# Optimization experiments

Measured on AMD Instinct MI355X. Metric: run time of the kernel, lower is better.

The kernel has to match this reference:

```python
import jax, jax.numpy as jnp
import numpy as np

EPS = 1e-5

def layernorm(x, g, b):
    mu = jnp.mean(x, axis=-1, keepdims=True)
    var = jnp.mean(jnp.square(x - mu), axis=-1, keepdims=True)
    return (x - mu) * jax.lax.rsqrt(var + EPS) * g + b

def rope(x):
    # x: [B, H, S, hd]; faithful to source: theta = 10000**(-2*pos/hd), pos in {0,2,4,...}
    S, hd = x.shape[-2], x.shape[-1]
    pos2 = jnp.arange(0, hd, 2, dtype=jnp.float32)
    theta = jnp.power(10000.0, -2.0 * pos2 / hd)          # [hd/2]
    ang = jnp.arange(S, dtype=jnp.float32)[:, None] * theta  # [S, hd/2]
    cos, sin = jnp.cos(ang), jnp.sin(ang)                  # broadcast over B,H
    xr = x.reshape(*x.shape[:-1], hd // 2, 2)
    x0, x1 = xr[..., 0], xr[..., 1]
    out = jnp.stack([x0 * cos - x1 * sin, x1 * cos + x0 * sin], axis=-1)
    return out.reshape(x.shape)

def setup_inputs() -> dict:
    key = jax.random.key(0)
    ks = jax.random.split(key, 8)
    B, S, D, H = 2, 2048, 1024, 16
    hd = D // H
    s_in = 1.0 / np.sqrt(D)
    s_h = 1.0 / np.sqrt(2 * D)
    return {
        "x": jax.random.normal(ks[0], (B, S, D), jnp.float32),
        "ln1_g": jnp.ones((D,), jnp.float32),
        "ln1_b": jnp.zeros((D,), jnp.float32),
        "Wq": jax.random.normal(ks[1], (H, D, hd), jnp.float32) * s_in,
        "Wk": jax.random.normal(ks[2], (H, D, hd), jnp.float32) * s_in,
        "Wv": jax.random.normal(ks[3], (H, D, hd), jnp.float32) * s_in,
        "Wo": jax.random.normal(ks[4], (D, D), jnp.float32) * s_in,
        "ln2_g": jnp.ones((D,), jnp.float32),
        "ln2_b": jnp.zeros((D,), jnp.float32),
        "W1": jax.random.normal(ks[5], (D, 2 * D), jnp.float32) * s_in,
        "W2": jax.random.normal(ks[6], (D, 2 * D), jnp.float32) * s_in,
        "W3": jax.random.normal(ks[7], (2 * D, D), jnp.float32) * s_h,
    }

def reference(x, ln1_g, ln1_b, Wq, Wk, Wv, Wo, ln2_g, ln2_b, W1, W2, W3):
    B, S, D = x.shape
    # --- attention sublayer ---
    h = layernorm(x, ln1_g, ln1_b)
    q = jnp.einsum("bsd,hdk->bhsk", h, Wq)
    k = jnp.einsum("bsd,hdk->bhsk", h, Wk)
    v = jnp.einsum("bsd,hdk->bhsk", h, Wv)
    q, k = rope(q), rope(k)
    hd = q.shape[-1]
    scores = jnp.einsum("bhqk,bhsk->bhqs", q, k) * (hd ** -0.5)  # [B,H,S,S]
    causal = jnp.tril(jnp.ones((S, S), bool))
    scores = jnp.where(causal, scores, jnp.float32(-jnp.inf))
    attn = jax.nn.softmax(scores, axis=-1)
    o = jnp.einsum("bhqs,bhsk->bhqk", attn, v)                   # [B,H,S,hd]
    o = o.transpose(0, 2, 1, 3).reshape(B, S, D)                 # concat heads
    x = x + o @ Wo
    # --- SwiGLU FFN sublayer ---
    h2 = layernorm(x, ln2_g, ln2_b)
    u = h2 @ W1
    ffn = (u * jax.nn.sigmoid(u)) * (h2 @ W2)
    return x + ffn @ W3
```

## Files before the change

### kernel.cpp

```cpp
#include <hip/hip_runtime.h>
#include <hip/hip_bf16.h>

using bf16 = __hip_bfloat16;
typedef __attribute__((ext_vector_type(8))) short bf16x8;
typedef __attribute__((ext_vector_type(4))) float f32x4;


__device__ inline float toF(float x) { return x; }
__device__ inline float toF(bf16 x) { return __bfloat162float(x); }
__device__ inline void  stV(float* p, float v) { *p = v; }
__device__ inline void  stV(bf16* p, float v) { *p = __float2bfloat16(v); }

__device__ __forceinline__ void unpack8(uint4 u, float* f) {
    f[0] = __uint_as_float(u.x << 16); f[1] = __uint_as_float(u.x & 0xffff0000u);
    f[2] = __uint_as_float(u.y << 16); f[3] = __uint_as_float(u.y & 0xffff0000u);
    f[4] = __uint_as_float(u.z << 16); f[5] = __uint_as_float(u.z & 0xffff0000u);
    f[6] = __uint_as_float(u.w << 16); f[7] = __uint_as_float(u.w & 0xffff0000u);
}

__device__ __forceinline__ uint4 packbf8(const float* f) {
    union { unsigned short u[8]; uint4 v; } r;
#pragma unroll
    for (int i = 0; i < 8; i++) {
        bf16 b = __float2bfloat16(f[i]);
        r.u[i] = *(unsigned short*)&b;
    }
    return r.v;
}

__device__ __forceinline__ unsigned pack2(float lo, float hi) {
    bf16 a = __float2bfloat16(lo), b = __float2bfloat16(hi);
    return ((unsigned)*(unsigned short*)&b << 16) | (unsigned)*(unsigned short*)&a;
}

__device__ __forceinline__ void gl_lds16(const void* g, void* l) {
    __builtin_amdgcn_global_load_lds(
        (__attribute__((address_space(1))) void*)g,
        (__attribute__((address_space(3))) void*)l, 16, 0, 0);
}

template <typename Tx, typename To>
__global__ __launch_bounds__(256) void ln_kernel(
    const Tx* __restrict__ x, const float* __restrict__ g,
    const float* __restrict__ b, To* __restrict__ out)
{
    const int D = 1024;
    int row = blockIdx.x;
    int tid = threadIdx.x;
    const Tx* xr = x + (size_t)row * D;

    float vals[4];
    float sum = 0.f, sumsq = 0.f;
#pragma unroll
    for (int i = 0; i < 4; i++) {
        float v = toF(xr[tid + i * 256]);
        vals[i] = v; sum += v; sumsq += v * v;
    }
#pragma unroll
    for (int off = 32; off > 0; off >>= 1) {
        sum += __shfl_xor(sum, off);
        sumsq += __shfl_xor(sumsq, off);
    }
    __shared__ float s1[4], s2[4];
    int wave = tid >> 6, lane = tid & 63;
    if (lane == 0) { s1[wave] = sum; s2[wave] = sumsq; }
    __syncthreads();
    sum = s1[0] + s1[1] + s1[2] + s1[3];
    sumsq = s2[0] + s2[1] + s2[2] + s2[3];

    float mu = sum * (1.f / D);
    float var = sumsq * (1.f / D) - mu * mu;
    float rstd = rsqrtf(var + 1e-5f);

    To* orow = out + (size_t)row * D;
#pragma unroll
    for (int i = 0; i < 4; i++) {
        int c = tid + i * 256;
        stV(&orow[c], (vals[i] - mu) * rstd * g[c] + b[c]);
    }
}

__global__ __launch_bounds__(256) void tconv_kernel(
    const float* __restrict__ in, bf16* __restrict__ out, int R, int C)
{
    __shared__ float t[32][33];
    int hh = blockIdx.z;
    const float* ip = in + (size_t)hh * R * C;
    bf16* op = out + (size_t)hh * R * C;
    int c0 = blockIdx.x * 32, r0 = blockIdx.y * 32;
    int tx = threadIdx.x & 31, ty = threadIdx.x >> 5;
#pragma unroll
    for (int i = 0; i < 4; i++)
        t[ty + 8 * i][tx] = ip[(size_t)(r0 + ty + 8 * i) * C + c0 + tx];
    __syncthreads();
#pragma unroll
    for (int i = 0; i < 4; i++)
        op[(size_t)(c0 + ty + 8 * i) * R + r0 + tx] = __float2bfloat16(t[tx][ty + 8 * i]);
}

__global__ __launch_bounds__(256) void tconv_w_kernel(
    const float* __restrict__ Aq, const float* __restrict__ Ak,
    const float* __restrict__ Av, const float* __restrict__ Ao,
    bf16* __restrict__ out)
{
    __shared__ float t[32][33];
    int z = blockIdx.z;
    const float* ip; int ldi;
    if (z < 48) {
        const float* s = (z < 16) ? Aq : (z < 32) ? Ak : Av;
        ip = s + (size_t)(z & 15) * 65536; ldi = 64;
    } else {
        ip = Ao + (size_t)(z - 48) * 64; ldi = 1024;
    }
    bf16* op = out + ((size_t)z << 16);
    int c0 = blockIdx.x * 32, r0 = blockIdx.y * 32;
    int tx = threadIdx.x & 31, ty = threadIdx.x >> 5;
#pragma unroll
    for (int i = 0; i < 4; i++)
        t[ty + 8 * i][tx] = ip[(size_t)(r0 + ty + 8 * i) * ldi + c0 + tx];
    __syncthreads();
#pragma unroll
    for (int i = 0; i < 4; i++)
        op[(size_t)(c0 + ty + 8 * i) * 1024 + r0 + tx] = __float2bfloat16(t[tx][ty + 8 * i]);
}

__global__ __launch_bounds__(256) void tconv12_kernel(
    const float* __restrict__ W1, const float* __restrict__ W2,
    bf16* __restrict__ out)
{
    __shared__ float t[32][33];
    int z = blockIdx.z;
    const float* ip = z ? W2 : W1;
    bf16* op = out + ((size_t)z << 21);
    int c0 = blockIdx.x * 32, r0 = blockIdx.y * 32;
    int tx = threadIdx.x & 31, ty = threadIdx.x >> 5;
#pragma unroll
    for (int i = 0; i < 4; i++)
        t[ty + 8 * i][tx] = ip[(size_t)(r0 + ty + 8 * i) * 2048 + c0 + tx];
    __syncthreads();
#pragma unroll
    for (int i = 0; i < 4; i++)
        op[(size_t)(c0 + ty + 8 * i) * 1024 + r0 + tx] = __float2bfloat16(t[tx][ty + 8 * i]);
}

template <int MODE>
__global__ __launch_bounds__(256) void mfma_gemm(
    const bf16* __restrict__ A, const bf16* __restrict__ BT0,
    void* __restrict__ Cv, const void* __restrict__ resv,
    int M, int N, int K)
{
    constexpr int NB = (MODE == 5) ? 3 : 2;
    __shared__ bf16 smem[2][NB][64 * 64];
    int tid = threadIdx.x, lane = tid & 63, w = tid >> 6;
    int wm = w >> 1, wn = w & 1;
    int m0 = blockIdx.y * 64, n0 = blockIdx.x * 64;

    const bf16* BT = BT0;
    bf16* Cq = nullptr; int rope = 0;
    if (MODE == 1) {
        int z = blockIdx.z;
        BT = BT0 + ((size_t)z << 20);
        Cq = (bf16*)Cv + ((size_t)z << 21);
        rope = (z < 2);
    }

    int lrow = lane >> 3;
    int lcb  = (lane & 7) ^ lrow;
    const bf16* Ag  = A  + (size_t)(m0 + w * 8 + lrow) * K + lcb * 8;
    const bf16* Bg0 = BT + (size_t)(n0 + w * 8 + lrow) * K + lcb * 8;
    const bf16* B2g = (MODE == 5)
        ? (const bf16*)resv + (size_t)(n0 + w * 8 + lrow) * K + lcb * 8
        : nullptr;
    unsigned sbase = (unsigned)__builtin_amdgcn_readfirstlane(w * 8 * 128);
    char* smc = (char*)smem;

    f32x4 acc[2][2], acc2[2][2];
#pragma unroll
    for (int i = 0; i < 2; i++)
#pragma unroll
        for (int j = 0; j < 2; j++) {
            acc[i][j] = (f32x4){0.f, 0.f, 0.f, 0.f};
            if (MODE == 5) acc2[i][j] = (f32x4){0.f, 0.f, 0.f, 0.f};
        }

    int cidx = lane & 15, quad = lane >> 4;

    auto STAGE = [&](int buf, int k0) {
        char* p = smc + (size_t)buf * (NB * 8192) + sbase;
        gl_lds16(Ag + k0,                   p);
        gl_lds16(Ag + (size_t)32 * K + k0,  p + 4096);
        gl_lds16(Bg0 + k0,                  p + 8192);
        gl_lds16(Bg0 + (size_t)32 * K + k0, p + 12288);
        if (MODE == 5) {
            gl_lds16(B2g + k0,                  p + 16384);
            gl_lds16(B2g + (size_t)32 * K + k0, p + 20480);
        }
    };

    STAGE(0, 0);
    __syncthreads();
    int cur = 0;
    for (int k0 = 0; k0 < K; k0 += 64) {
        if (k0 + 64 < K) STAGE(cur ^ 1, k0 + 64);
        const bf16* Ab = (const bf16*)(smc + (size_t)cur * (NB * 8192));
        const bf16* Bb = Ab + 4096;
        const bf16* B2b = Ab + 8192;
#pragma unroll
        for (int kk = 0; kk < 2; kk++) {
            int pb = (kk * 4 + quad) ^ (cidx & 7);
            bf16x8 af[2], bfr[2], b2f[2];
#pragma unroll
            for (int i = 0; i < 2; i++)
                af[i] = *(const bf16x8*)&Ab[(wm * 32 + i * 16 + cidx) * 64 + pb * 8];
#pragma unroll
            for (int j = 0; j < 2; j++)
                bfr[j] = *(const bf16x8*)&Bb[(wn * 32 + j * 16 + cidx) * 64 + pb * 8];
            if (MODE == 5) {
#pragma unroll
                for (int j = 0; j < 2; j++)
                    b2f[j] = *(const bf16x8*)&B2b[(wn * 32 + j * 16 + cidx) * 64 + pb * 8];
            }
            __builtin_amdgcn_s_setprio(1);
#pragma unroll
            for (int i = 0; i < 2; i++)
#pragma unroll
                for (int j = 0; j < 2; j++) {
                    acc[i][j] = __builtin_amdgcn_mfma_f32_16x16x32_bf16(af[i], bfr[j], acc[i][j], 0, 0, 0);
                    if (MODE == 5)
                        acc2[i][j] = __builtin_amdgcn_mfma_f32_16x16x32_bf16(af[i], b2f[j], acc2[i][j], 0, 0, 0);
                }
            __builtin_amdgcn_s_setprio(0);
        }
        __syncthreads();
        cur ^= 1;
    }

    int rbase = quad * 4;
#pragma unroll
    for (int i = 0; i < 2; i++) {
#pragma unroll
        for (int j = 0; j < 2; j++) {
            int row0 = m0 + wm * 32 + i * 16 + rbase;
            int col = n0 + wn * 32 + j * 16 + cidx;
            if (MODE == 1 && !rope) {
                int h_ = col >> 6, d = col & 63;
                uint2 t;
                t.x = pack2(acc[i][j][0], acc[i][j][1]);
                t.y = pack2(acc[i][j][2], acc[i][j][3]);
                *(uint2*)&Cq[(size_t)h_ * 131072 + (size_t)d * 2048 + row0] = t;
                continue;
            }
#pragma unroll
            for (int r = 0; r < 4; r++) {
                int row = row0 + r;
                float v = acc[i][j][r];
                size_t idx = (size_t)row * N + col;
                if (MODE == 1) {
                    int h_ = col >> 6, kk = col & 63;
                    float other = __shfl_xor(v, 1);
                    float p = (float)(kk >> 1);
                    float theta = __expf(p * -0.5756462732485114f);
                    float ang = (float)row * theta;
                    float c, sn; __sincosf(ang, &sn, &c);
                    float outv = (kk & 1) ? (v * c + other * sn) : (v * c - other * sn);
                    Cq[((size_t)h_ * 2048 + row) * 64 + kk] = __float2bfloat16(outv);
                } else if (MODE == 2) {
                    v += ((const float*)resv)[idx];
                    ((bf16*)Cv)[idx] = __float2bfloat16(v);
                } else if (MODE == 5) {
                    float g2 = acc2[i][j][r];
                    float sg = 1.f / (1.f + __expf(-v));
                    ((bf16*)Cv)[idx] = __float2bfloat16(v * sg * g2);
                } else {
                    v += __bfloat162float(((const bf16*)resv)[idx]);
                    ((float*)Cv)[idx] = v;
                }
            }
        }
    }
}

__global__ __launch_bounds__(256) void attn_kernel(
    const bf16* __restrict__ q, const bf16* __restrict__ k,
    const bf16* __restrict__ vt, bf16* __restrict__ o)
{
    const int S = 2048;
    __shared__ bf16 Ks[64][72];
    __shared__ bf16 Vs[64][72];
    __shared__ __align__(16) char QPbuf[64 * 72 * 2];

    int h = blockIdx.y;
    int qt = (h & 8) ? (int)blockIdx.x : 31 - (int)blockIdx.x;
    int tid = threadIdx.x, lane = tid & 63, w = tid >> 6;
    int quad = lane >> 4, cidx = lane & 15;
    int m0 = qt * 64;

    const bf16* qb = q + ((size_t)h * S + m0) * 64;
    const bf16* kb = k + (size_t)h * S * 64;
    const bf16* vtb = vt + (size_t)h * 64 * S;

    int srow = tid >> 2;
    int sg = (tid & 3) * 16;

    bf16 (*Qs)[72] = (bf16 (*)[72])QPbuf;
    {
        const uint4* src = (const uint4*)(qb + (size_t)srow * 64 + sg);
        uint4 u0 = src[0], u1 = src[1];
        float f[16]; unpack8(u0, f); unpack8(u1, f + 8);
#pragma unroll
        for (int i = 0; i < 16; i++) f[i] *= 0.125f * 1.44269504f;
        *(uint4*)&Qs[srow][sg] = packbf8(f);
        *(uint4*)&Qs[srow][sg + 8] = packbf8(f + 8);
    }
    bf16x8 bQ0 = *(const bf16x8*)&Qs[w * 16 + cidx][quad * 8];
    bf16x8 bQ1 = *(const bf16x8*)&Qs[w * 16 + cidx][32 + quad * 8];

    unsigned* Pst = (unsigned*)QPbuf + w * 576;

    float m_i = -INFINITY, l_i = 0.f;
    f32x4 Oc[4];
#pragma unroll
    for (int i = 0; i < 4; i++) Oc[i] = (f32x4){0.f, 0.f, 0.f, 0.f};

    uint4 ka0, ka1, va0, va1;
    {
        const uint4* ksrc = (const uint4*)(kb + (size_t)srow * 64 + sg);
        ka0 = ksrc[0]; ka1 = ksrc[1];
        const uint4* vsrc = (const uint4*)(vtb + (size_t)srow * S + sg);
        va0 = vsrc[0]; va1 = vsrc[1];
    }

    for (int kt = 0; kt <= qt; kt++) {
        __syncthreads();
        *(uint4*)&Ks[srow][sg] = ka0; *(uint4*)&Ks[srow][sg + 8] = ka1;
        *(uint4*)&Vs[srow][sg] = va0; *(uint4*)&Vs[srow][sg + 8] = va1;
        __syncthreads();
        if (kt < qt) {
            const uint4* kn = (const uint4*)(kb + (size_t)((kt + 1) * 64 + srow) * 64 + sg);
            ka0 = kn[0]; ka1 = kn[1];
            const uint4* vn = (const uint4*)(vtb + (size_t)srow * S + (kt + 1) * 64 + sg);
            va0 = vn[0]; va1 = vn[1];
        }

        f32x4 sc[4];
#pragma unroll
        for (int i = 0; i < 4; i++) {
            bf16x8 aK0 = *(const bf16x8*)&Ks[i * 16 + cidx][quad * 8];
            bf16x8 aK1 = *(const bf16x8*)&Ks[i * 16 + cidx][32 + quad * 8];
            f32x4 z = (f32x4){0.f, 0.f, 0.f, 0.f};
            z = __builtin_amdgcn_mfma_f32_16x16x32_bf16(aK0, bQ0, z, 0, 0, 0);
            z = __builtin_amdgcn_mfma_f32_16x16x32_bf16(aK1, bQ1, z, 0, 0, 0);
            sc[i] = z;
        }

        if (kt == qt) {
#pragma unroll
            for (int i = 0; i < 4; i++)
#pragma unroll
                for (int r = 0; r < 4; r++)
                    if (i * 16 + quad * 4 + r > w * 16 + cidx) sc[i][r] = -INFINITY;
        }

        float pmax = sc[0][0];
#pragma unroll
        for (int i = 0; i < 4; i++)
#pragma unroll
            for (int r = 0; r < 4; r++) pmax = fmaxf(pmax, sc[i][r]);
        pmax = fmaxf(pmax, __shfl_xor(pmax, 16));
        pmax = fmaxf(pmax, __shfl_xor(pmax, 32));
        float mnew = fmaxf(m_i, pmax);
        float alpha = __builtin_amdgcn_exp2f(m_i - mnew);
        float rs = 0.f;
#pragma unroll
        for (int i = 0; i < 4; i++)
#pragma unroll
            for (int r = 0; r < 4; r++) {
                sc[i][r] = __builtin_amdgcn_exp2f(sc[i][r] - mnew);
                rs += sc[i][r];
            }
        rs += __shfl_xor(rs, 16);
        rs += __shfl_xor(rs, 32);
        l_i = l_i * alpha + rs;
        m_i = mnew;
#pragma unroll
        for (int i = 0; i < 4; i++) {
            Oc[i][0] *= alpha; Oc[i][1] *= alpha;
            Oc[i][2] *= alpha; Oc[i][3] *= alpha;
        }

#pragma unroll
        for (int i = 0; i < 4; i++) {
            uint2 t;
            t.x = pack2(sc[i][0], sc[i][1]);
            t.y = pack2(sc[i][2], sc[i][3]);
            *(uint2*)&Pst[cidx * 36 + 8 * i + 2 * quad] = t;
        }
        bf16x8 bP0 = *(const bf16x8*)&Pst[cidx * 36 + 4 * quad];
        bf16x8 bP1 = *(const bf16x8*)&Pst[cidx * 36 + 16 + 4 * quad];

#pragma unroll
        for (int i = 0; i < 4; i++) {
            bf16x8 aV0 = *(const bf16x8*)&Vs[i * 16 + cidx][quad * 8];
            bf16x8 aV1 = *(const bf16x8*)&Vs[i * 16 + cidx][32 + quad * 8];
            Oc[i] = __builtin_amdgcn_mfma_f32_16x16x32_bf16(aV0, bP0, Oc[i], 0, 0, 0);
            Oc[i] = __builtin_amdgcn_mfma_f32_16x16x32_bf16(aV1, bP1, Oc[i], 0, 0, 0);
        }
    }

    float inv = 1.f / l_i;
#pragma unroll
    for (int i = 0; i < 4; i++) {
        uint2 t;
        t.x = pack2(Oc[i][0] * inv, Oc[i][1] * inv);
        t.y = pack2(Oc[i][2] * inv, Oc[i][3] * inv);
        *(uint2*)&Pst[cidx * 36 + 8 * i + 2 * quad] = t;
    }
    int r2 = lane >> 2, g2 = (lane & 3) * 8;
    uint4 o0 = *(const uint4*)&Pst[r2 * 36 + g2];
    uint4 o1 = *(const uint4*)&Pst[r2 * 36 + g2 + 4];
    bf16* orow = o + (size_t)(m0 + w * 16 + r2) * 1024 + h * 64;
    *(uint4*)(orow + g2 * 2) = o0;
    *(uint4*)(orow + g2 * 2 + 8) = o1;
}

extern "C" void kernel_launch(void* const* d_in, const int* in_sizes, int n_in,
                              void* d_out, int out_size, void* d_ws, size_t ws_size,
                              hipStream_t stream)
{
    const int S = 2048, D = 1024;

    const float* x    = (const float*)d_in[0];
    const float* ln1g = (const float*)d_in[1];
    const float* ln1b = (const float*)d_in[2];
    const float* Wq   = (const float*)d_in[3];
    const float* Wk   = (const float*)d_in[4];
    const float* Wv   = (const float*)d_in[5];
    const float* Wo   = (const float*)d_in[6];
    const float* ln2g = (const float*)d_in[7];
    const float* ln2b = (const float*)d_in[8];
    const float* W1   = (const float*)d_in[9];
    const float* W2   = (const float*)d_in[10];
    const float* W3   = (const float*)d_in[11];
    float* out = (float*)d_out;

    const size_t NR = (size_t)S * D;
    bf16* r0 = (bf16*)d_ws;
    bf16* r1 = r0 + NR;
    bf16* r2 = r1 + NR;
    bf16* r3 = r2 + NR;
    const size_t M1 = 1u << 20;

    for (int b = 0; b < 2; b++) {
        const float* xb = x + (size_t)b * S * D;
        float* ob = out + (size_t)b * S * D;
        bf16* pb = (bf16*)ob;

        ln_kernel<float, bf16><<<S, 256, 0, stream>>>(xb, ln1g, ln1b, r3);

        tconv_w_kernel<<<dim3(2, 32, 64), 256, 0, stream>>>(Wq, Wk, Wv, Wo, pb);

        mfma_gemm<1><<<dim3(16, 32, 3), 256, 0, stream>>>(r3, pb, r0, nullptr, S, 1024, 1024);

        attn_kernel<<<dim3(32, 16), 256, 0, stream>>>(r0, r1, r2, pb);

        mfma_gemm<2><<<dim3(16, 32, 1), 256, 0, stream>>>(pb, pb + 3 * M1, r3, xb, S, 1024, 1024);

        ln_kernel<bf16, bf16><<<S, 256, 0, stream>>>(r3, ln2g, ln2b, r0);

        tconv12_kernel<<<dim3(64, 32, 2), 256, 0, stream>>>(W1, W2, pb);

        mfma_gemm<5><<<dim3(32, 32, 1), 256, 0, stream>>>(r0, pb, r1, pb + 2 * M1, S, 2048, 1024);

        tconv_kernel<<<dim3(32, 64, 1), 256, 0, stream>>>(W3, r0, 2048, 1024);

        mfma_gemm<4><<<dim3(16, 32, 1), 256, 0, stream>>>(r1, r0, ob, r3, S, 1024, 2048);
    }
}
```

Before: 368.9 us.

## Widen attention key tile to 128 and fuse layernorm with weight conversion

The attention kernel now handles 128 keys per iteration instead of 64. This doubles the K/V shared-memory tiles and the P staging buffer, roughly halves the loop trip count and the barriers per query tile, and still applies the causal mask on the last tile. Separately, each layernorm launch is merged with its weight transpose/convert launch into one kernel that picks its role by block index, cutting the launch count. The costs are more shared memory per attention block, which may lower occupancy, and some masked waste on the final 128-wide tile for query tiles with even index.

```diff
diff --git a/kernel.cpp b/kernel.cpp
--- a/kernel.cpp
+++ b/kernel.cpp
@@ -8,8 +8,6 @@
 
 __device__ inline float toF(float x) { return x; }
 __device__ inline float toF(bf16 x) { return __bfloat162float(x); }
-__device__ inline void  stV(float* p, float v) { *p = v; }
-__device__ inline void  stV(bf16* p, float v) { *p = __float2bfloat16(v); }
 
 __device__ __forceinline__ void unpack8(uint4 u, float* f) {
     f[0] = __uint_as_float(u.x << 16); f[1] = __uint_as_float(u.x & 0xffff0000u);
@@ -39,13 +37,13 @@
         (__attribute__((address_space(3))) void*)l, 16, 0, 0);
 }
 
-template <typename Tx, typename To>
-__global__ __launch_bounds__(256) void ln_kernel(
+template <typename Tx>
+__device__ __forceinline__ void ln_body(
     const Tx* __restrict__ x, const float* __restrict__ g,
-    const float* __restrict__ b, To* __restrict__ out)
+    const float* __restrict__ b, bf16* __restrict__ out, int row,
+    float* s1, float* s2)
 {
     const int D = 1024;
-    int row = blockIdx.x;
     int tid = threadIdx.x;
     const Tx* xr = x + (size_t)row * D;
 
@@ -61,7 +59,6 @@
         sum += __shfl_xor(sum, off);
         sumsq += __shfl_xor(sumsq, off);
     }
-    __shared__ float s1[4], s2[4];
     int wave = tid >> 6, lane = tid & 63;
     if (lane == 0) { s1[wave] = sum; s2[wave] = sumsq; }
     __syncthreads();
@@ -72,21 +69,84 @@
     float var = sumsq * (1.f / D) - mu * mu;
     float rstd = rsqrtf(var + 1e-5f);
 
-    To* orow = out + (size_t)row * D;
+    bf16* orow = out + (size_t)row * D;
 #pragma unroll
     for (int i = 0; i < 4; i++) {
         int c = tid + i * 256;
-        stV(&orow[c], (vals[i] - mu) * rstd * g[c] + b[c]);
-    }
+        orow[c] = __float2bfloat16((vals[i] - mu) * rstd * g[c] + b[c]);
+    }
+}
+
+__global__ __launch_bounds__(256) void prep1_kernel(
+    const float* __restrict__ x, const float* __restrict__ g,
+    const float* __restrict__ b, bf16* __restrict__ h,
+    const float* __restrict__ Wq, const float* __restrict__ Wk,
+    const float* __restrict__ Wv, const float* __restrict__ Wo,
+    bf16* __restrict__ wt)
+{
+    __shared__ float t[32][33];
+    __shared__ float s1[4], s2[4];
+    int bx = blockIdx.x;
+    if (bx < 2048) {
+        ln_body<float>(x, g, b, h, bx, s1, s2);
+        return;
+    }
+    int zz = bx - 2048;
+    int z = zz >> 6, rem = zz & 63;
+    int yy = rem >> 1, xx = rem & 1;
+    const float* ip; int ldi;
+    if (z < 48) {
+        const float* s = (z < 16) ? Wq : (z < 32) ? Wk : Wv;
+        ip = s + (size_t)(z & 15) * 65536; ldi = 64;
+    } else {
+        ip = Wo + (size_t)(z - 48) * 64; ldi = 1024;
+    }
+    bf16* op = wt + ((size_t)z << 16);
+    int c0 = xx * 32, r0 = yy * 32;
+    int tx = threadIdx.x & 31, ty = threadIdx.x >> 5;
+#pragma unroll
+    for (int i = 0; i < 4; i++)
+        t[ty + 8 * i][tx] = ip[(size_t)(r0 + ty + 8 * i) * ldi + c0 + tx];
+    __syncthreads();
+#pragma unroll
+    for (int i = 0; i < 4; i++)
+        op[(size_t)(c0 + ty + 8 * i) * 1024 + r0 + tx] = __float2bfloat16(t[tx][ty + 8 * i]);
+}
+
+__global__ __launch_bounds__(256) void prep2_kernel(
+    const bf16* __restrict__ x2, const float* __restrict__ g,
+    const float* __restrict__ b, bf16* __restrict__ h2,
+    const float* __restrict__ W1, const float* __restrict__ W2,
+    bf16* __restrict__ wt)
+{
+    __shared__ float t[32][33];
+    __shared__ float s1[4], s2[4];
+    int bx = blockIdx.x;
+    if (bx < 2048) {
+        ln_body<bf16>(x2, g, b, h2, bx, s1, s2);
+        return;
+    }
+    int zz = bx - 2048;
+    int xx = zz & 63, yy = (zz >> 6) & 31, z = zz >> 11;
+    const float* ip = z ? W2 : W1;
+    bf16* op = wt + ((size_t)z << 21);
+    int c0 = xx * 32, r0 = yy * 32;
+    int tx = threadIdx.x & 31, ty = threadIdx.x >> 5;
+#pragma unroll
+    for (int i = 0; i < 4; i++)
+        t[ty + 8 * i][tx] = ip[(size_t)(r0 + ty + 8 * i) * 2048 + c0 + tx];
+    __syncthreads();
+#pragma unroll
+    for (int i = 0; i < 4; i++)
+        op[(size_t)(c0 + ty + 8 * i) * 1024 + r0 + tx] = __float2bfloat16(t[tx][ty + 8 * i]);
 }
 
 __global__ __launch_bounds__(256) void tconv_kernel(
     const float* __restrict__ in, bf16* __restrict__ out, int R, int C)
 {
     __shared__ float t[32][33];
-    int hh = blockIdx.z;
-    const float* ip = in + (size_t)hh * R * C;
-    bf16* op = out + (size_t)hh * R * C;
+    const float* ip = in;
+    bf16* op = out;
     int c0 = blockIdx.x * 32, r0 = blockIdx.y * 32;
     int tx = threadIdx.x & 31, ty = threadIdx.x >> 5;
 #pragma unroll
@@ -96,51 +156,6 @@
 #pragma unroll
     for (int i = 0; i < 4; i++)
         op[(size_t)(c0 + ty + 8 * i) * R + r0 + tx] = __float2bfloat16(t[tx][ty + 8 * i]);
-}
-
-__global__ __launch_bounds__(256) void tconv_w_kernel(
-    const float* __restrict__ Aq, const float* __restrict__ Ak,
-    const float* __restrict__ Av, const float* __restrict__ Ao,
-    bf16* __restrict__ out)
-{
-    __shared__ float t[32][33];
-    int z = blockIdx.z;
-    const float* ip; int ldi;
-    if (z < 48) {
-        const float* s = (z < 16) ? Aq : (z < 32) ? Ak : Av;
-        ip = s + (size_t)(z & 15) * 65536; ldi = 64;
-    } else {
-        ip = Ao + (size_t)(z - 48) * 64; ldi = 1024;
-    }
-    bf16* op = out + ((size_t)z << 16);
-    int c0 = blockIdx.x * 32, r0 = blockIdx.y * 32;
-    int tx = threadIdx.x & 31, ty = threadIdx.x >> 5;
-#pragma unroll
-    for (int i = 0; i < 4; i++)
-        t[ty + 8 * i][tx] = ip[(size_t)(r0 + ty + 8 * i) * ldi + c0 + tx];
-    __syncthreads();
-#pragma unroll
-    for (int i = 0; i < 4; i++)
-        op[(size_t)(c0 + ty + 8 * i) * 1024 + r0 + tx] = __float2bfloat16(t[tx][ty + 8 * i]);
-}
-
-__global__ __launch_bounds__(256) void tconv12_kernel(
-    const float* __restrict__ W1, const float* __restrict__ W2,
-    bf16* __restrict__ out)
-{
-    __shared__ float t[32][33];
-    int z = blockIdx.z;
-    const float* ip = z ? W2 : W1;
-    bf16* op = out + ((size_t)z << 21);
-    int c0 = blockIdx.x * 32, r0 = blockIdx.y * 32;
-    int tx = threadIdx.x & 31, ty = threadIdx.x >> 5;
-#pragma unroll
-    for (int i = 0; i < 4; i++)
-        t[ty + 8 * i][tx] = ip[(size_t)(r0 + ty + 8 * i) * 2048 + c0 + tx];
-    __syncthreads();
-#pragma unroll
-    for (int i = 0; i < 4; i++)
-        op[(size_t)(c0 + ty + 8 * i) * 1024 + r0 + tx] = __float2bfloat16(t[tx][ty + 8 * i]);
 }
 
 template <int MODE>
@@ -285,9 +300,9 @@
     const bf16* __restrict__ vt, bf16* __restrict__ o)
 {
     const int S = 2048;
-    __shared__ bf16 Ks[64][72];
-    __shared__ bf16 Vs[64][72];
-    __shared__ __align__(16) char QPbuf[64 * 72 * 2];
+    __shared__ bf16 Ks[128][72];
+    __shared__ bf16 Vs[64][136];
+    __shared__ __align__(16) char QPbuf[4 * 16 * 272];
 
     int h = blockIdx.y;
     int qt = (h & 8) ? (int)blockIdx.x : 31 - (int)blockIdx.x;
@@ -300,7 +315,8 @@
     const bf16* vtb = vt + (size_t)h * 64 * S;
 
     int srow = tid >> 2;
-    int sg = (tid & 3) * 16;
+    int sg  = (tid & 3) * 16;
+    int sg2 = (tid & 3) * 32;
 
     bf16 (*Qs)[72] = (bf16 (*)[72])QPbuf;
     {
@@ -315,36 +331,42 @@
     bf16x8 bQ0 = *(const bf16x8*)&Qs[w * 16 + cidx][quad * 8];
     bf16x8 bQ1 = *(const bf16x8*)&Qs[w * 16 + cidx][32 + quad * 8];
 
-    unsigned* Pst = (unsigned*)QPbuf + w * 576;
+    unsigned* Pst = (unsigned*)QPbuf + w * (16 * 68);
 
     float m_i = -INFINITY, l_i = 0.f;
     f32x4 Oc[4];
 #pragma unroll
     for (int i = 0; i < 4; i++) Oc[i] = (f32x4){0.f, 0.f, 0.f, 0.f};
 
-    uint4 ka0, ka1, va0, va1;
+    int nt = qt / 2 + 1;
+
+    uint4 ka[4], va[4];
     {
-        const uint4* ksrc = (const uint4*)(kb + (size_t)srow * 64 + sg);
-        ka0 = ksrc[0]; ka1 = ksrc[1];
-        const uint4* vsrc = (const uint4*)(vtb + (size_t)srow * S + sg);
-        va0 = vsrc[0]; va1 = vsrc[1];
-    }
-
-    for (int kt = 0; kt <= qt; kt++) {
+        const uint4* k0 = (const uint4*)(kb + (size_t)srow * 64 + sg);
+        const uint4* k1 = (const uint4*)(kb + (size_t)(srow + 64) * 64 + sg);
+        ka[0] = k0[0]; ka[1] = k0[1]; ka[2] = k1[0]; ka[3] = k1[1];
+        const uint4* v0 = (const uint4*)(vtb + (size_t)srow * S + sg2);
+        va[0] = v0[0]; va[1] = v0[1]; va[2] = v0[2]; va[3] = v0[3];
+    }
+
+    for (int kt = 0; kt < nt; kt++) {
         __syncthreads();
-        *(uint4*)&Ks[srow][sg] = ka0; *(uint4*)&Ks[srow][sg + 8] = ka1;
-        *(uint4*)&Vs[srow][sg] = va0; *(uint4*)&Vs[srow][sg + 8] = va1;
+        *(uint4*)&Ks[srow][sg] = ka[0];      *(uint4*)&Ks[srow][sg + 8] = ka[1];
+        *(uint4*)&Ks[srow + 64][sg] = ka[2]; *(uint4*)&Ks[srow + 64][sg + 8] = ka[3];
+        *(uint4*)&Vs[srow][sg2] = va[0];     *(uint4*)&Vs[srow][sg2 + 8] = va[1];
+        *(uint4*)&Vs[srow][sg2 + 16] = va[2];*(uint4*)&Vs[srow][sg2 + 24] = va[3];
         __syncthreads();
-        if (kt < qt) {
-            const uint4* kn = (const uint4*)(kb + (size_t)((kt + 1) * 64 + srow) * 64 + sg);
-            ka0 = kn[0]; ka1 = kn[1];
-            const uint4* vn = (const uint4*)(vtb + (size_t)srow * S + (kt + 1) * 64 + sg);
-            va0 = vn[0]; va1 = vn[1];
-        }
-
-        f32x4 sc[4];
-#pragma unroll
-        for (int i = 0; i < 4; i++) {
+        if (kt + 1 < nt) {
+            const uint4* k0 = (const uint4*)(kb + (size_t)((kt + 1) * 128 + srow) * 64 + sg);
+            const uint4* k1 = (const uint4*)(kb + (size_t)((kt + 1) * 128 + srow + 64) * 64 + sg);
+            ka[0] = k0[0]; ka[1] = k0[1]; ka[2] = k1[0]; ka[3] = k1[1];
+            const uint4* v0 = (const uint4*)(vtb + (size_t)srow * S + (kt + 1) * 128 + sg2);
+            va[0] = v0[0]; va[1] = v0[1]; va[2] = v0[2]; va[3] = v0[3];
+        }
+
+        f32x4 sc[8];
+#pragma unroll
+        for (int i = 0; i < 8; i++) {
             bf16x8 aK0 = *(const bf16x8*)&Ks[i * 16 + cidx][quad * 8];
             bf16x8 aK1 = *(const bf16x8*)&Ks[i * 16 + cidx][32 + quad * 8];
             f32x4 z = (f32x4){0.f, 0.f, 0.f, 0.f};
@@ -353,17 +375,18 @@
             sc[i] = z;
         }
 
-        if (kt == qt) {
-#pragma unroll
-            for (int i = 0; i < 4; i++)
+        if (kt == nt - 1) {
+            int qpos = m0 + w * 16 + cidx;
+#pragma unroll
+            for (int i = 0; i < 8; i++)
 #pragma unroll
                 for (int r = 0; r < 4; r++)
-                    if (i * 16 + quad * 4 + r > w * 16 + cidx) sc[i][r] = -INFINITY;
-        }
-
-        float pmax = sc[0][0];
-#pragma unroll
-        for (int i = 0; i < 4; i++)
+                    if (kt * 128 + i * 16 + quad * 4 + r > qpos) sc[i][r] = -INFINITY;
+        }
+
+        float pmax = -INFINITY;
+#pragma unroll
+        for (int i = 0; i < 8; i++)
 #pragma unroll
             for (int r = 0; r < 4; r++) pmax = fmaxf(pmax, sc[i][r]);
         pmax = fmaxf(pmax, __shfl_xor(pmax, 16));
@@ -372,7 +395,7 @@
         float alpha = __builtin_amdgcn_exp2f(m_i - mnew);
         float rs = 0.f;
 #pragma unroll
-        for (int i = 0; i < 4; i++)
+        for (int i = 0; i < 8; i++)
 #pragma unroll
             for (int r = 0; r < 4; r++) {
                 sc[i][r] = __builtin_amdgcn_exp2f(sc[i][r] - mnew);
@@ -389,22 +412,24 @@
         }
 
 #pragma unroll
-        for (int i = 0; i < 4; i++) {
+        for (int i = 0; i < 8; i++) {
             uint2 t;
             t.x = pack2(sc[i][0], sc[i][1]);
             t.y = pack2(sc[i][2], sc[i][3]);
-            *(uint2*)&Pst[cidx * 36 + 8 * i + 2 * quad] = t;
-        }
-        bf16x8 bP0 = *(const bf16x8*)&Pst[cidx * 36 + 4 * quad];
-        bf16x8 bP1 = *(const bf16x8*)&Pst[cidx * 36 + 16 + 4 * quad];
-
-#pragma unroll
-        for (int i = 0; i < 4; i++) {
-            bf16x8 aV0 = *(const bf16x8*)&Vs[i * 16 + cidx][quad * 8];
-            bf16x8 aV1 = *(const bf16x8*)&Vs[i * 16 + cidx][32 + quad * 8];
-            Oc[i] = __builtin_amdgcn_mfma_f32_16x16x32_bf16(aV0, bP0, Oc[i], 0, 0, 0);
-            Oc[i] = __builtin_amdgcn_mfma_f32_16x16x32_bf16(aV1, bP1, Oc[i], 0, 0, 0);
-        }
+            *(uint2*)&Pst[cidx * 68 + 8 * i + 2 * quad] = t;
+        }
+        bf16x8 bP[4];
+#pragma unroll
+        for (int ks = 0; ks < 4; ks++)
+            bP[ks] = *(const bf16x8*)&Pst[cidx * 68 + 16 * ks + 4 * quad];
+
+#pragma unroll
+        for (int i = 0; i < 4; i++)
+#pragma unroll
+            for (int ks = 0; ks < 4; ks++) {
+                bf16x8 aV = *(const bf16x8*)&Vs[i * 16 + cidx][ks * 32 + quad * 8];
+                Oc[i] = __builtin_amdgcn_mfma_f32_16x16x32_bf16(aV, bP[ks], Oc[i], 0, 0, 0);
+            }
     }
 
     float inv = 1.f / l_i;
@@ -413,11 +438,11 @@
         uint2 t;
         t.x = pack2(Oc[i][0] * inv, Oc[i][1] * inv);
         t.y = pack2(Oc[i][2] * inv, Oc[i][3] * inv);
-        *(uint2*)&Pst[cidx * 36 + 8 * i + 2 * quad] = t;
+        *(uint2*)&Pst[cidx * 68 + 8 * i + 2 * quad] = t;
     }
     int r2 = lane >> 2, g2 = (lane & 3) * 8;
-    uint4 o0 = *(const uint4*)&Pst[r2 * 36 + g2];
-    uint4 o1 = *(const uint4*)&Pst[r2 * 36 + g2 + 4];
+    uint4 o0 = *(const uint4*)&Pst[r2 * 68 + g2];
+    uint4 o1 = *(const uint4*)&Pst[r2 * 68 + g2 + 4];
     bf16* orow = o + (size_t)(m0 + w * 16 + r2) * 1024 + h * 64;
     *(uint4*)(orow + g2 * 2) = o0;
     *(uint4*)(orow + g2 * 2 + 8) = o1;
@@ -455,9 +480,8 @@
         float* ob = out + (size_t)b * S * D;
         bf16* pb = (bf16*)ob;
 
-        ln_kernel<float, bf16><<<S, 256, 0, stream>>>(xb, ln1g, ln1b, r3);
-
-        tconv_w_kernel<<<dim3(2, 32, 64), 256, 0, stream>>>(Wq, Wk, Wv, Wo, pb);
+        prep1_kernel<<<6144, 256, 0, stream>>>(xb, ln1g, ln1b, r3,
+                                               Wq, Wk, Wv, Wo, pb);
 
         mfma_gemm<1><<<dim3(16, 32, 3), 256, 0, stream>>>(r3, pb, r0, nullptr, S, 1024, 1024);
 
@@ -465,13 +489,11 @@
 
         mfma_gemm<2><<<dim3(16, 32, 1), 256, 0, stream>>>(pb, pb + 3 * M1, r3, xb, S, 1024, 1024);
 
-        ln_kernel<bf16, bf16><<<S, 256, 0, stream>>>(r3, ln2g, ln2b, r0);
-
-        tconv12_kernel<<<dim3(64, 32, 2), 256, 0, stream>>>(W1, W2, pb);
+        prep2_kernel<<<6144, 256, 0, stream>>>(r3, ln2g, ln2b, r0, W1, W2, pb);
 
         mfma_gemm<5><<<dim3(32, 32, 1), 256, 0, stream>>>(r0, pb, r1, pb + 2 * M1, S, 2048, 1024);
 
-        tconv_kernel<<<dim3(32, 64, 1), 256, 0, stream>>>(W3, r0, 2048, 1024);
+        tconv_kernel<<<dim3(32, 64), 256, 0, stream>>>(W3, r0, 2048, 1024);
 
         mfma_gemm<4><<<dim3(16, 32, 1), 256, 0, stream>>>(r1, r0, ob, r3, S, 1024, 2048);
     }
```

After: 419.3 us. 1.14x slower.
